# Performance work log

Measured on AMD Instinct MI355X. Metric: run time of the kernel, lower is better.

Reference implementation:

```python
import jax, jax.numpy as jnp
import numpy as np

D_MODEL, N_HEAD, D_HEAD = 1024, 16, 64
BATCH, Q_LEN = 2, 2048
LN_EPS = 1e-5


def _rel_shift(x):
    # x: [b, q, k, n] -- standard Transformer-XL relative shift
    b, q, k, n = x.shape
    zero_pad = jnp.zeros((b, q, 1, n), dtype=x.dtype)
    x_padded = jnp.concatenate([zero_pad, x], axis=2)      # [b, q, k+1, n]
    x_padded = x_padded.reshape(b, k + 1, q, n)
    return x_padded[:, 1:].reshape(b, q, k, n)


def _layer_norm(x, gamma, beta):
    mu = jnp.mean(x, axis=-1, keepdims=True)
    var = jnp.mean(jnp.square(x - mu), axis=-1, keepdims=True)
    return (x - mu) * jax.lax.rsqrt(var + LN_EPS) * gamma + beta


def setup_inputs() -> dict:
    key = jax.random.key(0)
    ks = jax.random.split(key, 8)
    inp = {
        "x": jax.random.normal(ks[0], (BATCH, Q_LEN, D_MODEL), jnp.float32),
        "relative_pos": jax.random.normal(ks[1], (Q_LEN, D_MODEL), jnp.float32),
        "r_w_bias": jax.random.normal(ks[2], (N_HEAD, D_HEAD), jnp.float32) * 0.02,
        "r_r_bias": jax.random.normal(ks[3], (N_HEAD, D_HEAD), jnp.float32) * 0.02,
        "attn_mask": jax.random.randint(ks[4], (BATCH, Q_LEN), 0, 2).astype(bool),
        "W_qkv": jax.random.normal(ks[5], (D_MODEL, 3 * N_HEAD * D_HEAD), jnp.float32) / np.sqrt(D_MODEL),
        "W_rel": jax.random.normal(ks[6], (D_MODEL, N_HEAD * D_HEAD), jnp.float32) / np.sqrt(D_MODEL),
        "W_out": jax.random.normal(ks[7], (N_HEAD * D_HEAD, D_MODEL), jnp.float32) / np.sqrt(N_HEAD * D_HEAD),
        "ln_gamma": jnp.ones((D_MODEL,), jnp.float32),
        "ln_beta": jnp.zeros((D_MODEL,), jnp.float32),
    }
    return inp


def reference(x, relative_pos, r_w_bias, r_r_bias, attn_mask, W_qkv, W_rel, W_out, ln_gamma, ln_beta):
    b, q_len, _ = x.shape
    r_len = relative_pos.shape[0]
    scale = 1.0 / np.sqrt(D_HEAD)

    w_heads = x @ W_qkv                                    # [b, q, 3*n*d]
    w_q, w_k, w_v = jnp.split(w_heads, 3, axis=-1)
    k_len = w_k.shape[1]

    w_q = w_q.reshape(b, q_len, N_HEAD, D_HEAD)
    w_k = w_k.reshape(b, k_len, N_HEAD, D_HEAD)
    w_v = w_v.reshape(b, k_len, N_HEAD, D_HEAD)
    r_k = (relative_pos @ W_rel).reshape(r_len, N_HEAD, D_HEAD)

    rw_q = w_q + r_w_bias                                  # [b, q, n, d]
    rr_q = w_q + r_r_bias

    ac = jnp.einsum('bind,bjnd->bijn', rw_q, w_k)          # content score
    bd = jnp.einsum('bind,jnd->bijn', rr_q, r_k)           # position score
    bd = _rel_shift(bd)

    attn_score = (ac + bd) * scale                         # [b, q, k, n]
    attn_score = jnp.where(attn_mask[:, None, :, None], -jnp.inf, attn_score)
    attn_prob = jax.nn.softmax(attn_score, axis=2)

    context = jnp.einsum('bijn,bjnd->bind', attn_prob, w_v)
    context = context.reshape(b, q_len, N_HEAD * D_HEAD)
    attn_out = context @ W_out
    return _layer_norm(x + attn_out, ln_gamma, ln_beta)
```

## Files before the change

kernel.cpp:

```cpp
#include <hip/hip_runtime.h>
#include <hip/hip_bf16.h>
#include <math.h>

#define S_LEN 2048
#define NHEAD 16
#define DHEAD 64
#define DMODEL 1024
#define NBATCH 2

typedef unsigned short u16;
typedef __attribute__((ext_vector_type(8))) short bf16x8;
typedef __attribute__((ext_vector_type(4))) short short4v;
typedef __attribute__((ext_vector_type(4))) float f32x4;

__device__ __forceinline__ short f2bs(float x) {
    __hip_bfloat16 h = __float2bfloat16(x);
    return __builtin_bit_cast(short, h);
}

#define GL2LDS(g, l)                                                         \
    __builtin_amdgcn_global_load_lds(                                        \
        (const __attribute__((address_space(1))) void*)(g),                  \
        (__attribute__((address_space(3))) void*)(l), 16, 0, 0)

__global__ __launch_bounds__(256) void cast_f32_bf16(const float* __restrict__ in,
                                                     u16* __restrict__ out) {
    const int i = (blockIdx.x * 256 + threadIdx.x) * 4;
    float4 v = *(const float4*)(in + i);
    short4v t;
    t[0] = f2bs(v.x); t[1] = f2bs(v.y); t[2] = f2bs(v.z); t[3] = f2bs(v.w);
    *(short4v*)(out + i) = t;
}

__global__ __launch_bounds__(256) void transp_cast(const float* __restrict__ W,
                                                   u16* __restrict__ Wt,
                                                   int K, int N) {
    __shared__ float t[64][65];
    const int k0 = blockIdx.y * 64, n0 = blockIdx.x * 64;
    const int r = threadIdx.x >> 4;
    const int c4 = (threadIdx.x & 15) * 4;
    #pragma unroll
    for (int it = 0; it < 4; ++it) {
        float4 v = *(const float4*)(W + (size_t)(k0 + it * 16 + r) * N + n0 + c4);
        t[c4 + 0][it * 16 + r] = v.x;
        t[c4 + 1][it * 16 + r] = v.y;
        t[c4 + 2][it * 16 + r] = v.z;
        t[c4 + 3][it * 16 + r] = v.w;
    }
    __syncthreads();
    #pragma unroll
    for (int it = 0; it < 4; ++it) {
        const int nn = it * 16 + r;
        short4v o;
        o[0] = f2bs(t[nn][c4 + 0]); o[1] = f2bs(t[nn][c4 + 1]);
        o[2] = f2bs(t[nn][c4 + 2]); o[3] = f2bs(t[nn][c4 + 3]);
        *(short4v*)(Wt + (size_t)(n0 + nn) * K + k0 + c4) = o;
    }
}

#define GEMM_BODY(Aptr, Btptr, Kdim)                                          \
    __shared__ u16 As[128 * 64];                                              \
    __shared__ u16 Bs[128 * 64];                                              \
    const int tid = threadIdx.x;                                              \
    const int lane = tid & 63;                                                \
    const int w = tid >> 6;                                                   \
    const int quad = lane >> 4, col = lane & 15;                              \
    const int bm = blockIdx.y * 128, bn = blockIdx.x * 128;                   \
    const int wm = (w >> 1) * 64, wn = (w & 1) * 64;                          \
    f32x4 acc[4][4];                                                          \
    _Pragma("unroll")                                                         \
    for (int mt = 0; mt < 4; ++mt)                                            \
        _Pragma("unroll")                                                     \
        for (int nt = 0; nt < 4; ++nt) acc[mt][nt] = (f32x4){0.f,0.f,0.f,0.f};\
    for (int k0 = 0; k0 < (Kdim); k0 += 64) {                                 \
        _Pragma("unroll")                                                     \
        for (int it = 0; it < 4; ++it) {                                      \
            const int cb = it * 256 + w * 64;                                 \
            const int c = cb + lane;                                          \
            const int r = c >> 3;                                             \
            const int o = ((c & 7) ^ (r & 7)) * 8;                            \
            GL2LDS((Aptr) + (size_t)(bm + r) * (Kdim) + k0 + o, As + (size_t)cb * 8); \
            GL2LDS((Btptr) + (size_t)(bn + r) * (Kdim) + k0 + o, Bs + (size_t)cb * 8);\
        }                                                                     \
        __syncthreads();                                                      \
        _Pragma("unroll")                                                     \
        for (int kc = 0; kc < 2; ++kc) {                                      \
            bf16x8 af[4], bfr[4];                                             \
            _Pragma("unroll")                                                 \
            for (int t = 0; t < 4; ++t) {                                     \
                const int am = wm + t * 16 + col;                             \
                const int aj = kc * 4 + quad;                                 \
                af[t] = *(const bf16x8*)&As[(size_t)am * 64 + ((aj ^ (am & 7)) * 8)]; \
                const int bn2 = wn + t * 16 + col;                            \
                bfr[t] = *(const bf16x8*)&Bs[(size_t)bn2 * 64 + ((aj ^ (bn2 & 7)) * 8)]; \
            }                                                                 \
            _Pragma("unroll")                                                 \
            for (int mt = 0; mt < 4; ++mt)                                    \
                _Pragma("unroll")                                             \
                for (int nt = 0; nt < 4; ++nt)                                \
                    acc[mt][nt] = __builtin_amdgcn_mfma_f32_16x16x32_bf16(    \
                        af[mt], bfr[nt], acc[mt][nt], 0, 0, 0);               \
        }                                                                     \
        __syncthreads();                                                      \
    }

__global__ __launch_bounds__(256, 2) void gemm_qkv(
    const u16* __restrict__ A, const u16* __restrict__ Bt,
    const float* __restrict__ rwb, const float* __restrict__ rrb,
    u16* __restrict__ qrw_b, u16* __restrict__ qrr_b,
    u16* __restrict__ kb, u16* __restrict__ vbT)
{
    GEMM_BODY(A, Bt, DMODEL)
    #pragma unroll
    for (int mt = 0; mt < 4; ++mt) {
        const int row0 = bm + wm + mt * 16 + quad * 4;
        const int b = row0 >> 11;
        const int s0 = row0 & 2047;
        #pragma unroll
        for (int nt = 0; nt < 4; ++nt) {
            const int cn = bn + wn + nt * 16 + col;
            const int sec = cn >> 10;
            const int cc = cn & 1023;
            const int h = cc >> 6, d = cc & 63;
            const int bh = b * NHEAD + h;
            if (sec == 0) {
                const float bw = rwb[cc], br = rrb[cc];
                #pragma unroll
                for (int r = 0; r < 4; ++r) {
                    const size_t o = ((size_t)bh * S_LEN + s0 + r) * 64 + d;
                    qrw_b[o] = (u16)f2bs(acc[mt][nt][r] + bw);
                    qrr_b[o] = (u16)f2bs(acc[mt][nt][r] + br);
                }
            } else if (sec == 1) {
                #pragma unroll
                for (int r = 0; r < 4; ++r)
                    kb[((size_t)bh * S_LEN + s0 + r) * 64 + d] =
                        (u16)f2bs(acc[mt][nt][r]);
            } else {
                short4v t;
                t[0] = f2bs(acc[mt][nt][0]); t[1] = f2bs(acc[mt][nt][1]);
                t[2] = f2bs(acc[mt][nt][2]); t[3] = f2bs(acc[mt][nt][3]);
                *(short4v*)(vbT + ((size_t)bh * 64 + d) * S_LEN + s0) = t;
            }
        }
    }
}

__global__ __launch_bounds__(256, 2) void gemm_rel(
    const u16* __restrict__ A, const u16* __restrict__ Bt,
    u16* __restrict__ rkb)
{
    GEMM_BODY(A, Bt, DMODEL)
    #pragma unroll
    for (int mt = 0; mt < 4; ++mt) {
        const int l0 = bm + wm + mt * 16 + quad * 4;
        #pragma unroll
        for (int nt = 0; nt < 4; ++nt) {
            const int cn = bn + wn + nt * 16 + col;
            const int h = cn >> 6, d = cn & 63;
            #pragma unroll
            for (int r = 0; r < 4; ++r)
                rkb[((size_t)h * S_LEN + l0 + r) * 64 + d] =
                    (u16)f2bs(acc[mt][nt][r]);
        }
    }
}

__global__ __launch_bounds__(256, 2) void gemm_out(
    const u16* __restrict__ A, const u16* __restrict__ Bt,
    float* __restrict__ Cf, int N, int K)
{
    GEMM_BODY(A, Bt, K)
    #pragma unroll
    for (int mt = 0; mt < 4; ++mt)
        #pragma unroll
        for (int nt = 0; nt < 4; ++nt)
            #pragma unroll
            for (int r = 0; r < 4; ++r) {
                const int row = bm + wm + mt * 16 + quad * 4 + r;
                const int cn = bn + wn + nt * 16 + col;
                Cf[(size_t)row * N + cn] = acc[mt][nt][r];
            }
}

__global__ __launch_bounds__(512, 2) void flash_attn(
    const u16* __restrict__ qrw_b, const u16* __restrict__ qrr_b,
    const u16* __restrict__ kb, const u16* __restrict__ vbT,
    const u16* __restrict__ rkb, const int* __restrict__ mask,
    u16* __restrict__ ctxb)
{
    const int lane = threadIdx.x & 63;
    const int w    = threadIdx.x >> 6;
    const int quad = lane >> 4;
    const int col  = lane & 15;
    const int bh   = blockIdx.y;
    const int b    = bh >> 4;
    const int n    = bh & 15;
    const int B0   = blockIdx.x * 128;
    const int iw0  = B0 + w * 16;

    __shared__ u16 Ks[64 * 64];
    __shared__ u16 Vs[64 * 64];
    __shared__ u16 Rs[192 * 64];
    __shared__ u16 Pr[8][16][72];
    __shared__ float madd[S_LEN];

    const size_t headQ = (size_t)bh * S_LEN * 64;
    const size_t headR = (size_t)n  * S_LEN * 64;

    for (int i = threadIdx.x; i < S_LEN; i += 512)
        madd[i] = mask[b * S_LEN + i] ? -16384.f : 0.f;

    bf16x8 a_rw[2], a_rr0[2], a_rr1[2];
    {
        const int r0 = iw0 + col;
        const int r1 = (r0 + 1 < S_LEN) ? (r0 + 1) : (S_LEN - 1);
        #pragma unroll
        for (int kc = 0; kc < 2; ++kc) {
            const int doff = kc * 32 + quad * 8;
            a_rw[kc]  = *(const bf16x8*)(qrw_b + headQ + (size_t)r0 * 64 + doff);
            a_rr0[kc] = *(const bf16x8*)(qrr_b + headQ + (size_t)r0 * 64 + doff);
            a_rr1[kc] = *(const bf16x8*)(qrr_b + headQ + (size_t)r1 * 64 + doff);
        }
    }

    f32x4 O[4];
    float l_acc[4] = {0.f, 0.f, 0.f, 0.f};
    #pragma unroll
    for (int dt = 0; dt < 4; ++dt) O[dt] = (f32x4){0.f, 0.f, 0.f, 0.f};

    const int swz  = ((lane & 7) ^ ((lane >> 3) & 7)) * 8;
    const int lrow = lane >> 3;
    const int csel = col & 7;
    const int delta = B0 - 0 + 16 * w;

    for (int u0 = 0; u0 < S_LEN; u0 += 64) {
        const int dblk = B0 - u0;
        const int dw = dblk + 16 * w;
        const bool mixed = (dw >= 0) && (dw <= 48);
        __syncthreads();
        const int pbase = (dblk >= 0) ? (S_LEN - 128 - dblk) : (-dblk - 129);
        #pragma unroll
        for (int t = 0; t < 5; ++t) {
            const int idx = w * 5 + t;
            if (idx < 8) {
                GL2LDS(kb + headQ + (size_t)(u0 + idx * 8 + lrow) * 64 + swz,
                       Ks + idx * 512);
            } else if (idx < 16) {
                const int c = idx - 8;
                GL2LDS(vbT + ((size_t)bh * 64 + c * 8 + lrow) * S_LEN + u0 + swz,
                       Vs + c * 512);
            } else {
                const int c = idx - 16;
                int rr = pbase + c * 8 + lrow;
                rr = rr < 0 ? 0 : (rr > S_LEN - 1 ? S_LEN - 1 : rr);
                GL2LDS(rkb + headR + (size_t)rr * 64 + swz, Rs + c * 512);
            }
        }
        bf16x8 rf2[5][2];
        if (mixed) {
            #pragma unroll
            for (int g = 0; g < 5; ++g) {
                const int u = g * 16 + col;
                int row = (dblk >= 0) ? (u - dw - 17) : (S_LEN - 16 - dw + u);
                row = row < 0 ? 0 : (row > S_LEN - 1 ? S_LEN - 1 : row);
                const u16* rb = rkb + headR + (size_t)row * 64 + quad * 8;
                rf2[g][0] = *(const bf16x8*)(rb);
                rf2[g][1] = *(const bf16x8*)(rb + 32);
            }
        }
        __syncthreads();

        f32x4 sc[4];
        #pragma unroll
        for (int nt = 0; nt < 4; ++nt) {
            const int m = nt * 16 + col;
            bf16x8 k0 = *(const bf16x8*)&Ks[m * 64 + ((quad ^ csel) * 8)];
            bf16x8 k1 = *(const bf16x8*)&Ks[m * 64 + (((4 + quad) ^ csel) * 8)];
            f32x4 c = (f32x4){0.f, 0.f, 0.f, 0.f};
            c = __builtin_amdgcn_mfma_f32_16x16x32_bf16(a_rw[0], k0, c, 0, 0, 0);
            c = __builtin_amdgcn_mfma_f32_16x16x32_bf16(a_rw[1], k1, c, 0, 0, 0);
            sc[nt] = c;
        }

        f32x4 pnl[5], oth[5];
        {
            const bf16x8* aP = (dblk >= 0) ? a_rr0 : a_rr1;
            #pragma unroll
            for (int g = 0; g < 5; ++g) {
                const int m = g * 16 + col + 112 - 16 * w;
                bf16x8 r0 = *(const bf16x8*)&Rs[m * 64 + ((quad ^ csel) * 8)];
                bf16x8 r1 = *(const bf16x8*)&Rs[m * 64 + (((4 + quad) ^ csel) * 8)];
                f32x4 c = (f32x4){0.f, 0.f, 0.f, 0.f};
                c = __builtin_amdgcn_mfma_f32_16x16x32_bf16(aP[0], r0, c, 0, 0, 0);
                c = __builtin_amdgcn_mfma_f32_16x16x32_bf16(aP[1], r1, c, 0, 0, 0);
                pnl[g] = c;
            }
        }
        #pragma unroll
        for (int g = 0; g < 5; ++g) oth[g] = (f32x4){0.f, 0.f, 0.f, 0.f};
        if (mixed) {
            const bf16x8* aV = (dblk >= 0) ? a_rr1 : a_rr0;
            #pragma unroll
            for (int g = 0; g < 5; ++g) {
                f32x4 c = (f32x4){0.f, 0.f, 0.f, 0.f};
                c = __builtin_amdgcn_mfma_f32_16x16x32_bf16(aV[0], rf2[g][0], c, 0, 0, 0);
                c = __builtin_amdgcn_mfma_f32_16x16x32_bf16(aV[1], rf2[g][1], c, 0, 0, 0);
                oth[g] = c;
            }
        }
        const int lim1 = 15 + dw;
        #pragma unroll
        for (int g = 0; g < 5; ++g) {
            const int u = g * 16 + col;
            #pragma unroll
            for (int r = 0; r < 4; ++r) {
                const float r1v = (dblk >= 0) ? pnl[g][r] : oth[g][r];
                const float r2v = (dblk >= 0) ? oth[g][r] : pnl[g][r];
                pnl[g][r] = (u <= lim1) ? r1v : ((u == lim1 + 1) ? 0.f : r2v);
            }
        }

        #pragma unroll
        for (int nt = 0; nt < 4; ++nt) {
            const float ma = madd[u0 + nt * 16 + col];
            #pragma unroll
            for (int r = 0; r < 4; ++r) {
                const int uo = col + 15 - quad * 4 - r;
                const int src = (quad << 4) | (uo & 15);
                float blo = __shfl(pnl[nt][r], src, 64);
                float bhi = __shfl(pnl[nt + 1][r], src, 64);
                float bd = (uo < 16) ? blo : bhi;
                float p = __expf(fmaf(sc[nt][r] + bd, 0.125f, ma));
                sc[nt][r] = p;
                l_acc[r] += p;
            }
        }

        #pragma unroll
        for (int nt = 0; nt < 4; ++nt)
            #pragma unroll
            for (int r = 0; r < 4; ++r)
                Pr[w][quad * 4 + r][nt * 16 + col] = (u16)f2bs(sc[nt][r]);
        bf16x8 pa[2];
        pa[0] = *(const bf16x8*)&Pr[w][col][quad * 8];
        pa[1] = *(const bf16x8*)&Pr[w][col][32 + quad * 8];

        #pragma unroll
        for (int dt = 0; dt < 4; ++dt) {
            const int m = dt * 16 + col;
            bf16x8 v0 = *(const bf16x8*)&Vs[m * 64 + ((quad ^ csel) * 8)];
            bf16x8 v1 = *(const bf16x8*)&Vs[m * 64 + (((4 + quad) ^ csel) * 8)];
            f32x4 c = O[dt];
            c = __builtin_amdgcn_mfma_f32_16x16x32_bf16(pa[0], v0, c, 0, 0, 0);
            c = __builtin_amdgcn_mfma_f32_16x16x32_bf16(pa[1], v1, c, 0, 0, 0);
            O[dt] = c;
        }
    }

    float inv[4];
    #pragma unroll
    for (int r = 0; r < 4; ++r) {
        float s = l_acc[r];
        #pragma unroll
        for (int off = 1; off < 16; off <<= 1)
            s += __shfl_xor(s, off, 64);
        inv[r] = 1.f / s;
    }
    #pragma unroll
    for (int dt = 0; dt < 4; ++dt)
        #pragma unroll
        for (int r = 0; r < 4; ++r) {
            const int i = iw0 + quad * 4 + r;
            ctxb[((size_t)b * S_LEN + i) * DMODEL + n * 64 + dt * 16 + col] =
                (u16)f2bs(O[dt][r] * inv[r]);
        }
}

__global__ __launch_bounds__(256) void ln_kernel(const float* __restrict__ x,
                                                 const float* __restrict__ ao,
                                                 const float* __restrict__ gamma,
                                                 const float* __restrict__ beta,
                                                 float* __restrict__ out) {
    const int r = blockIdx.x;
    const int tid = threadIdx.x;
    const size_t base = (size_t)r * DMODEL + tid * 4;
    float4 xv = *(const float4*)(x + base);
    float4 av = *(const float4*)(ao + base);
    float v0 = xv.x + av.x, v1 = xv.y + av.y, v2 = xv.z + av.z, v3 = xv.w + av.w;

    float s = v0 + v1 + v2 + v3;
    #pragma unroll
    for (int off = 32; off > 0; off >>= 1) s += __shfl_xor(s, off, 64);
    __shared__ float red[4];
    __shared__ float red2[4];
    if ((tid & 63) == 0) red[tid >> 6] = s;
    __syncthreads();
    float mu = (red[0] + red[1] + red[2] + red[3]) * (1.0f / DMODEL);

    float d0 = v0 - mu, d1 = v1 - mu, d2 = v2 - mu, d3 = v3 - mu;
    float q = d0 * d0 + d1 * d1 + d2 * d2 + d3 * d3;
    #pragma unroll
    for (int off = 32; off > 0; off >>= 1) q += __shfl_xor(q, off, 64);
    if ((tid & 63) == 0) red2[tid >> 6] = q;
    __syncthreads();
    float var = (red2[0] + red2[1] + red2[2] + red2[3]) * (1.0f / DMODEL);
    float rstd = rsqrtf(var + 1e-5f);

    float4 g  = *(const float4*)(gamma + tid * 4);
    float4 be = *(const float4*)(beta + tid * 4);
    float4 o = make_float4(d0 * rstd * g.x + be.x,
                           d1 * rstd * g.y + be.y,
                           d2 * rstd * g.z + be.z,
                           d3 * rstd * g.w + be.w);
    *(float4*)(out + base) = o;
}

extern "C" void kernel_launch(void* const* d_in, const int* in_sizes, int n_in,
                              void* d_out, int out_size, void* d_ws, size_t ws_size,
                              hipStream_t stream) {
    const float* x    = (const float*)d_in[0];
    const float* rpos = (const float*)d_in[1];
    const float* rwb  = (const float*)d_in[2];
    const float* rrb  = (const float*)d_in[3];
    const int*   mask = (const int*)  d_in[4];
    const float* Wqkv = (const float*)d_in[5];
    const float* Wrel = (const float*)d_in[6];
    const float* Wout = (const float*)d_in[7];
    const float* gam  = (const float*)d_in[8];
    const float* bet  = (const float*)d_in[9];
    float* out = (float*)d_out;

    u16* wsb   = (u16*)d_ws;
    u16* ctxb  = wsb;
    float* ao  = (float*)(wsb + 4194304);
    u16* qrw_b = wsb + 12582912;
    u16* qrr_b = qrw_b + 4194304;
    u16* kb    = qrr_b + 4194304;
    u16* vbT   = kb + 4194304;
    u16* rkb   = vbT + 4194304;
    u16* xb    = rkb + 2097152;
    u16* rposb = xb + 4194304;
    u16* Wqkvt = rposb + 2097152;
    u16* Wrelt = Wqkvt + 3145728;
    u16* Woutt = Wrelt + 1048576;

    dim3 blk(256);
    cast_f32_bf16<<<dim3(4096), blk, 0, stream>>>(x, xb);
    transp_cast<<<dim3(48, 16), blk, 0, stream>>>(Wqkv, Wqkvt, DMODEL, 3 * DMODEL);
    gemm_qkv<<<dim3(24, 32), blk, 0, stream>>>(xb, Wqkvt, rwb, rrb,
                                               qrw_b, qrr_b, kb, vbT);
    cast_f32_bf16<<<dim3(2048), blk, 0, stream>>>(rpos, rposb);
    transp_cast<<<dim3(16, 16), blk, 0, stream>>>(Wrel, Wrelt, DMODEL, DMODEL);
    gemm_rel<<<dim3(8, 16), blk, 0, stream>>>(rposb, Wrelt, rkb);
    transp_cast<<<dim3(16, 16), blk, 0, stream>>>(Wout, Woutt, DMODEL, DMODEL);
    flash_attn<<<dim3(S_LEN / 128, NBATCH * NHEAD), dim3(512), 0, stream>>>(
        qrw_b, qrr_b, kb, vbT, rkb, mask, ctxb);
    gemm_out<<<dim3(8, 32), blk, 0, stream>>>(ctxb, Woutt, ao, DMODEL, DMODEL);
    ln_kernel<<<dim3(NBATCH * S_LEN), blk, 0, stream>>>(x, ao, gam, bet, out);
}
```

Baseline: 350.2 us.

## Merge cast and transpose launches and streamline rel-shift select in attention

Folds the two f32-to-bf16 casts into one launch and the three weight transpose-casts into one launch, cutting the kernel count from ten to seven. Inside flash_attn, the rel-shift merge is moved into the mixed branch, so unmixed tiles skip the per-element select. A special case zeroes column 0 when dw == -16. The shuffles are also restructured so each pnl register is shuffled once and reused across adjacent tiles, which removes redundant cross-lane shuffles at the cost of some extra live registers.

```diff
diff --git a/kernel.cpp b/kernel.cpp
--- a/kernel.cpp
+++ b/kernel.cpp
@@ -23,20 +23,36 @@
         (const __attribute__((address_space(1))) void*)(g),                  \
         (__attribute__((address_space(3))) void*)(l), 16, 0, 0)
 
-__global__ __launch_bounds__(256) void cast_f32_bf16(const float* __restrict__ in,
-                                                     u16* __restrict__ out) {
-    const int i = (blockIdx.x * 256 + threadIdx.x) * 4;
+__global__ __launch_bounds__(256) void cast_all(const float* __restrict__ x,
+                                                const float* __restrict__ rpos,
+                                                u16* __restrict__ xb,
+                                                u16* __restrict__ rposb) {
+    int bid = blockIdx.x;
+    const float* in;
+    u16* out;
+    if (bid < 4096) { in = x; out = xb; }
+    else            { in = rpos; out = rposb; bid -= 4096; }
+    const int i = (bid * 256 + threadIdx.x) * 4;
     float4 v = *(const float4*)(in + i);
     short4v t;
     t[0] = f2bs(v.x); t[1] = f2bs(v.y); t[2] = f2bs(v.z); t[3] = f2bs(v.w);
     *(short4v*)(out + i) = t;
 }
 
-__global__ __launch_bounds__(256) void transp_cast(const float* __restrict__ W,
-                                                   u16* __restrict__ Wt,
-                                                   int K, int N) {
+__global__ __launch_bounds__(256) void transp_cast_all(
+    const float* __restrict__ Wqkv, const float* __restrict__ Wrel,
+    const float* __restrict__ Wout,
+    u16* __restrict__ Wqkvt, u16* __restrict__ Wrelt, u16* __restrict__ Woutt)
+{
     __shared__ float t[64][65];
-    const int k0 = blockIdx.y * 64, n0 = blockIdx.x * 64;
+    int bx = blockIdx.x;
+    const float* W;
+    u16* Wt;
+    int N;
+    if (bx < 48)      { W = Wqkv; Wt = Wqkvt; N = 3 * DMODEL; }
+    else if (bx < 64) { W = Wrel; Wt = Wrelt; N = DMODEL; bx -= 48; }
+    else              { W = Wout; Wt = Woutt; N = DMODEL; bx -= 64; }
+    const int k0 = blockIdx.y * 64, n0 = bx * 64;
     const int r = threadIdx.x >> 4;
     const int c4 = (threadIdx.x & 15) * 4;
     #pragma unroll
@@ -54,7 +70,7 @@
         short4v o;
         o[0] = f2bs(t[nn][c4 + 0]); o[1] = f2bs(t[nn][c4 + 1]);
         o[2] = f2bs(t[nn][c4 + 2]); o[3] = f2bs(t[nn][c4 + 3]);
-        *(short4v*)(Wt + (size_t)(n0 + nn) * K + k0 + c4) = o;
+        *(short4v*)(Wt + (size_t)(n0 + nn) * DMODEL + k0 + c4) = o;
     }
 }
 
@@ -232,7 +248,6 @@
     const int swz  = ((lane & 7) ^ ((lane >> 3) & 7)) * 8;
     const int lrow = lane >> 3;
     const int csel = col & 7;
-    const int delta = B0 - 0 + 16 * w;
 
     for (int u0 = 0; u0 < S_LEN; u0 += 64) {
         const int dblk = B0 - u0;
@@ -283,7 +298,7 @@
             sc[nt] = c;
         }
 
-        f32x4 pnl[5], oth[5];
+        f32x4 pnl[5];
         {
             const bf16x8* aP = (dblk >= 0) ? a_rr0 : a_rr1;
             #pragma unroll
@@ -297,41 +312,45 @@
                 pnl[g] = c;
             }
         }
-        #pragma unroll
-        for (int g = 0; g < 5; ++g) oth[g] = (f32x4){0.f, 0.f, 0.f, 0.f};
         if (mixed) {
             const bf16x8* aV = (dblk >= 0) ? a_rr1 : a_rr0;
+            const int lim1 = 15 + dw;
             #pragma unroll
             for (int g = 0; g < 5; ++g) {
                 f32x4 c = (f32x4){0.f, 0.f, 0.f, 0.f};
                 c = __builtin_amdgcn_mfma_f32_16x16x32_bf16(aV[0], rf2[g][0], c, 0, 0, 0);
                 c = __builtin_amdgcn_mfma_f32_16x16x32_bf16(aV[1], rf2[g][1], c, 0, 0, 0);
-                oth[g] = c;
-            }
-        }
-        const int lim1 = 15 + dw;
-        #pragma unroll
-        for (int g = 0; g < 5; ++g) {
-            const int u = g * 16 + col;
-            #pragma unroll
-            for (int r = 0; r < 4; ++r) {
-                const float r1v = (dblk >= 0) ? pnl[g][r] : oth[g][r];
-                const float r2v = (dblk >= 0) ? oth[g][r] : pnl[g][r];
-                pnl[g][r] = (u <= lim1) ? r1v : ((u == lim1 + 1) ? 0.f : r2v);
-            }
-        }
-
-        #pragma unroll
-        for (int nt = 0; nt < 4; ++nt) {
-            const float ma = madd[u0 + nt * 16 + col];
-            #pragma unroll
-            for (int r = 0; r < 4; ++r) {
-                const int uo = col + 15 - quad * 4 - r;
-                const int src = (quad << 4) | (uo & 15);
-                float blo = __shfl(pnl[nt][r], src, 64);
-                float bhi = __shfl(pnl[nt + 1][r], src, 64);
-                float bd = (uo < 16) ? blo : bhi;
-                float p = __expf(fmaf(sc[nt][r] + bd, 0.125f, ma));
+                const int u = g * 16 + col;
+                #pragma unroll
+                for (int r = 0; r < 4; ++r) {
+                    const float r1v = (dblk >= 0) ? pnl[g][r] : c[r];
+                    const float r2v = (dblk >= 0) ? c[r] : pnl[g][r];
+                    pnl[g][r] = (u <= lim1) ? r1v : ((u == lim1 + 1) ? 0.f : r2v);
+                }
+            }
+        } else if (dw == -16) {
+            if (col == 0) {
+                #pragma unroll
+                for (int r = 0; r < 4; ++r) pnl[0][r] = 0.f;
+            }
+        }
+
+        float madd_v[4];
+        #pragma unroll
+        for (int nt = 0; nt < 4; ++nt)
+            madd_v[nt] = madd[u0 + nt * 16 + col];
+        #pragma unroll
+        for (int r = 0; r < 4; ++r) {
+            const int uo = col + 15 - quad * 4 - r;
+            const int src = (quad << 4) | (uo & 15);
+            float rot[5];
+            #pragma unroll
+            for (int g = 0; g < 5; ++g)
+                rot[g] = __shfl(pnl[g][r], src, 64);
+            #pragma unroll
+            for (int nt = 0; nt < 4; ++nt) {
+                const float bd = (uo < 16) ? rot[nt] : rot[nt + 1];
+                const float p = __expf(fmaf(sc[nt][r] + bd, 0.125f, madd_v[nt]));
                 sc[nt][r] = p;
                 l_acc[r] += p;
             }
@@ -446,14 +465,12 @@
     u16* Woutt = Wrelt + 1048576;
 
     dim3 blk(256);
-    cast_f32_bf16<<<dim3(4096), blk, 0, stream>>>(x, xb);
-    transp_cast<<<dim3(48, 16), blk, 0, stream>>>(Wqkv, Wqkvt, DMODEL, 3 * DMODEL);
+    cast_all<<<dim3(6144), blk, 0, stream>>>(x, rpos, xb, rposb);
+    transp_cast_all<<<dim3(80, 16), blk, 0, stream>>>(Wqkv, Wrel, Wout,
+                                                      Wqkvt, Wrelt, Woutt);
     gemm_qkv<<<dim3(24, 32), blk, 0, stream>>>(xb, Wqkvt, rwb, rrb,
                                                qrw_b, qrr_b, kb, vbT);
-    cast_f32_bf16<<<dim3(2048), blk, 0, stream>>>(rpos, rposb);
-    transp_cast<<<dim3(16, 16), blk, 0, stream>>>(Wrel, Wrelt, DMODEL, DMODEL);
     gemm_rel<<<dim3(8, 16), blk, 0, stream>>>(rposb, Wrelt, rkb);
-    transp_cast<<<dim3(16, 16), blk, 0, stream>>>(Wout, Woutt, DMODEL, DMODEL);
     flash_attn<<<dim3(S_LEN / 128, NBATCH * NHEAD), dim3(512), 0, stream>>>(
         qrw_b, qrr_b, kb, vbT, rkb, mask, ctxb);
     gemm_out<<<dim3(8, 32), blk, 0, stream>>>(ctxb, Woutt, ao, DMODEL, DMODEL);
```

Measured after the change: 417.6 us. +19.2%, slower.
